# Optimization experiments

Measured on AMD Instinct MI355X. Metric: run time of the kernel, lower is better.

Reference implementation:

```python
import jax, jax.numpy as jnp
import numpy as np

B = 65536   # batch
F = 256     # FeatureDim
E = 8       # experts_num
D = 64      # ExpertOutDim
EPS = 1e-5  # BatchNorm eps (eval mode: running stats)


def _bn(x, g, be, m, v):
    # BatchNorm1d in eval mode
    return (x - m) * jax.lax.rsqrt(v + EPS) * g + be


def setup_inputs() -> dict:
    key = jax.random.key(0)
    ks = jax.random.split(key, 40)
    r = lambda i, s: jax.random.normal(ks[i], s, dtype=jnp.float32) * 0.05
    u = lambda i, s: jax.random.uniform(ks[i], s, dtype=jnp.float32)
    return dict(
        signal_em=jax.random.normal(ks[0], (B, F), dtype=jnp.float32),
        muti_em=jax.random.normal(ks[1], (B, F), dtype=jnp.float32),
        similarity=jax.random.uniform(ks[2], (B,), dtype=jnp.float32),
        w=u(3, ()), b=u(4, ()),
        ps_W=r(5, (F, 256)), ps_b=r(6, (256,)), ps_g=u(7, (256,)), ps_be=r(8, (256,)), ps_m=r(9, (256,)), ps_v=u(10, (256,)) + 0.5,
        pm_W=r(11, (F, 256)), pm_b=r(12, (256,)), pm_g=u(13, (256,)), pm_be=r(14, (256,)), pm_m=r(15, (256,)), pm_v=u(16, (256,)) + 0.5,
        c1_W=r(17, (2 * F, 64)), c1_b=r(18, (64,)), c1_g=u(19, (64,)), c1_be=r(20, (64,)), c1_m=r(21, (64,)), c1_v=u(22, (64,)) + 0.5,
        c2_W=r(23, (64, 64)), c2_b=r(24, (64,)), c2_g=u(25, (64,)), c2_be=r(26, (64,)), c2_m=r(27, (64,)), c2_v=u(28, (64,)) + 0.5,
        c3_W=r(29, (64, 2)), c3_b=r(30, (2,)),
        e_W1=r(31, (E, 2 * F, 256)), e_b1=r(32, (E, 256)),
        e_W2=r(33, (E, 256, D)), e_b2=r(34, (E, D)),
        s_W1=r(35, (E, E)), s_b1=r(36, (E,)), s_W2=r(37, (E, E)), s_b2=r(38, (E,)),
    )


def reference(signal_em, muti_em, similarity, w, b,
              ps_W, ps_b, ps_g, ps_be, ps_m, ps_v,
              pm_W, pm_b, pm_g, pm_be, pm_m, pm_v,
              c1_W, c1_b, c1_g, c1_be, c1_m, c1_v,
              c2_W, c2_b, c2_g, c2_be, c2_m, c2_v,
              c3_W, c3_b,
              e_W1, e_b1, e_W2, e_b2,
              s_W1, s_b1, s_W2, s_b2):
    sim_weight = similarity[:, None] * w + b                        # [B,1]
    sig = jax.nn.relu(_bn(signal_em @ ps_W + ps_b, ps_g, ps_be, ps_m, ps_v))
    sig = sim_weight * sig
    mut = jax.nn.relu(_bn(muti_em @ pm_W + pm_b, pm_g, pm_be, pm_m, pm_v))
    temp = jnp.concatenate([sig, mut], axis=1)                      # [B, 512]

    # classifier head (dropout = identity in eval mode)
    h = jax.nn.relu(_bn(temp @ c1_W + c1_b, c1_g, c1_be, c1_m, c1_v))
    h = jax.nn.relu(_bn(h @ c2_W + c2_b, c2_g, c2_be, c2_m, c2_v))
    pre_score = h @ c3_W + c3_b                                     # [B,2]

    # all E experts as one batched GEMM (Expert_net has dropout p=0)
    eh = jax.nn.relu(jnp.einsum('bf,efh->beh', temp, e_W1) + e_b1)  # [B,E,256]
    eo = jax.nn.relu(jnp.einsum('beh,ehd->bed', eh, e_W2) + e_b2)   # [B,E,64]

    # SE-style gating: avg/max pool over expert-out dim (kernel==D -> scalar)
    att_ave = eo.mean(axis=-1)                                      # [B,E]
    att_max = eo.max(axis=-1)                                       # [B,E]
    senet = lambda x: jax.nn.gelu(x @ s_W1 + s_b1, approximate=False) @ s_W2 + s_b2
    wts = jax.nn.sigmoid(senet(att_ave) + senet(att_max))           # [B,E]

    gate_out = jnp.einsum('bed,be->bd', eo, wts)                    # [B,D]
    return (gate_out, pre_score)
```

## Files before the change

### kernel.cpp

```cpp
#include <hip/hip_runtime.h>
#include <math.h>

using u32 = unsigned int;
using u16 = unsigned short;
typedef __attribute__((ext_vector_type(4))) float f4;
typedef __attribute__((ext_vector_type(4))) u32 u4;
typedef __attribute__((ext_vector_type(2))) u32 u2;
typedef __attribute__((ext_vector_type(8))) __bf16 b8;

union U4B8 { u4 u; b8 b; };

__device__ __forceinline__ u16 f2b(float x) {
  u32 u = __float_as_uint(x);
  u32 r = (u + 0x7FFFu + ((u >> 16) & 1u)) >> 16;
  return (u16)r;
}
__device__ __forceinline__ u32 pack2(float a, float b) { return (u32)f2b(a) | ((u32)f2b(b) << 16); }
__device__ __forceinline__ f4 mfma16(b8 a, b8 b, f4 c) {
  return __builtin_amdgcn_mfma_f32_16x16x32_bf16(a, b, c, 0, 0, 0);
}

#define FENCE() asm volatile("" ::: "memory")
#define RAWBAR() do { FENCE(); __builtin_amdgcn_s_barrier(); FENCE(); __builtin_amdgcn_sched_barrier(0); } while (0)
#define VMW(nlit) do { asm volatile("s_waitcnt vmcnt(" nlit ")" ::: "memory"); __builtin_amdgcn_sched_barrier(0); } while (0)
#define LGKM0() do { asm volatile("s_waitcnt lgkmcnt(0)" ::: "memory"); __builtin_amdgcn_sched_barrier(0); } while (0)
#define LBAR() do { LGKM0(); __builtin_amdgcn_s_barrier(); FENCE(); __builtin_amdgcn_sched_barrier(0); } while (0)

template <int NB>
__device__ __forceinline__ void gstage(const u16* g, u16* l, int t) {
#pragma unroll
  for (int i = 0; i < NB; i += 8192) {
    __builtin_amdgcn_global_load_lds(
        (__attribute__((address_space(1))) u32*)(g + (i >> 1) + t * 8),
        (__attribute__((address_space(3))) u32*)(l + (i >> 1) + ((t >> 6) << 9)),
        16, 0, 0);
  }
}

__global__ void prep_kernel(
    const float* __restrict__ ps_W, const float* __restrict__ ps_b, const float* __restrict__ ps_g,
    const float* __restrict__ ps_be, const float* __restrict__ ps_m, const float* __restrict__ ps_v,
    const float* __restrict__ pm_W, const float* __restrict__ pm_b, const float* __restrict__ pm_g,
    const float* __restrict__ pm_be, const float* __restrict__ pm_m, const float* __restrict__ pm_v,
    const float* __restrict__ c1_W, const float* __restrict__ c1_b, const float* __restrict__ c1_g,
    const float* __restrict__ c1_be, const float* __restrict__ c1_m, const float* __restrict__ c1_v,
    const float* __restrict__ c2_W, const float* __restrict__ c2_b, const float* __restrict__ c2_g,
    const float* __restrict__ c2_be, const float* __restrict__ c2_m, const float* __restrict__ c2_v,
    const float* __restrict__ e_W1, const float* __restrict__ e_W2,
    u16* __restrict__ w1t, u16* __restrict__ w2t, u16* __restrict__ pst, u16* __restrict__ pmt,
    u16* __restrict__ c1t, u16* __restrict__ c2t, float* __restrict__ fold)
{
  int i0 = blockIdx.x * blockDim.x + threadIdx.x;
  int stride = gridDim.x * blockDim.x;
  for (int idx = i0; idx < 8 * 256 * 512; idx += stride) {
    int e = idx >> 17; int rem = idx & 131071;
    int s = rem >> 14; int rem2 = rem & 16383;
    int n = rem2 >> 6; int q = rem2 & 63;
    int k = s * 64 + (q ^ ((n & 7) << 3));
    w1t[idx] = f2b(e_W1[e * 131072 + k * 256 + n]);
  }
  for (int idx = i0; idx < 8 * 64 * 256; idx += stride) {
    int e = idx >> 14; int rem = idx & 16383;
    int d = rem >> 8; int q = rem & 255;
    int h = q ^ ((d & 7) << 3);
    w2t[idx] = f2b(e_W2[e * 16384 + h * 64 + d]);
  }
  for (int idx = i0; idx < 65536; idx += stride) {
    int s = idx >> 14; int rem = idx & 16383;
    int n = rem >> 6, q = rem & 63;
    int k = s * 64 + (q ^ ((n & 7) << 3));
    pst[idx] = f2b(ps_W[k * 256 + n]);
    pmt[idx] = f2b(pm_W[k * 256 + n]);
  }
  for (int idx = i0; idx < 64 * 512; idx += stride) {
    int n = idx >> 9, q = idx & 511;
    int k = q ^ ((n & 7) << 3);
    c1t[idx] = f2b(c1_W[k * 64 + n]);
  }
  for (int idx = i0; idx < 64 * 64; idx += stride) {
    int n = idx >> 6, k = idx & 63;
    c2t[idx] = f2b(c2_W[k * 64 + n]);
  }
  for (int idx = i0; idx < 256; idx += stride) {
    float a = ps_g[idx] * rsqrtf(ps_v[idx] + 1e-5f);
    fold[idx] = a; fold[256 + idx] = (ps_b[idx] - ps_m[idx]) * a + ps_be[idx];
    float a2 = pm_g[idx] * rsqrtf(pm_v[idx] + 1e-5f);
    fold[512 + idx] = a2; fold[768 + idx] = (pm_b[idx] - pm_m[idx]) * a2 + pm_be[idx];
  }
  for (int idx = i0; idx < 64; idx += stride) {
    float a = c1_g[idx] * rsqrtf(c1_v[idx] + 1e-5f);
    fold[1024 + idx] = a; fold[1088 + idx] = (c1_b[idx] - c1_m[idx]) * a + c1_be[idx];
    float a2 = c2_g[idx] * rsqrtf(c2_v[idx] + 1e-5f);
    fold[1152 + idx] = a2; fold[1216 + idx] = (c2_b[idx] - c2_m[idx]) * a2 + c2_be[idx];
  }
}

__global__ __launch_bounds__(512, 4) void k1_kernel(
    const float* __restrict__ sig, const float* __restrict__ mut,
    const float* __restrict__ simil, const float* __restrict__ wS, const float* __restrict__ bS,
    const u16* __restrict__ pst, const u16* __restrict__ pmt,
    const float* __restrict__ fold, u16* __restrict__ temp)
{
  extern __shared__ __align__(16) u16 smk[];
  const int t = threadIdx.x, w = t >> 6, l = t & 63;
  const int lr = l & 15, lk = (l >> 4) * 8, lv = (l >> 4) * 4;
  const int xoru = (l & 7) << 3;
  const int rg = w >> 1, cg = w & 1;
  const int half = blockIdx.y;
  const float* X = half ? mut : sig;
  const u16* Wt = half ? pmt : pst;
  const int rb = blockIdx.x;
  const int rg0 = rb * 64;
  const f4 ZF = {0.f, 0.f, 0.f, 0.f};
  const int myrow = rg * 16 + lr;

  f4 xr[16];
  {
    const float* xp = X + (rg0 + myrow) * 256 + lk;
#pragma unroll
    for (int c = 0; c < 8; ++c) {
      xr[2 * c]     = *(const f4*)(xp + c * 32);
      xr[2 * c + 1] = *(const f4*)(xp + c * 32 + 4);
    }
  }
  float swv = 1.f;
  if (half == 0) swv = simil[rg0 + myrow] * wS[0] + bS[0];
  gstage<32768>(Wt, smk, t);
  b8 af[8];
#pragma unroll
  for (int c = 0; c < 8; ++c) {
    U4B8 tmp;
    tmp.u[0] = pack2(xr[2 * c][0], xr[2 * c][1]);
    tmp.u[1] = pack2(xr[2 * c][2], xr[2 * c][3]);
    tmp.u[2] = pack2(xr[2 * c + 1][0], xr[2 * c + 1][1]);
    tmp.u[3] = pack2(xr[2 * c + 1][2], xr[2 * c + 1][3]);
    af[c] = tmp.b;
  }

  f4 acc[8];
#pragma unroll
  for (int i = 0; i < 8; ++i) acc[i] = ZF;

#define K1P(P, STG) do { \
    VMW("0"); RAWBAR(); \
    STG; \
    __builtin_amdgcn_s_setprio(1); \
    _Pragma("unroll") for (int kk = 0; kk < 2; ++kk) { \
      b8 bf[8]; \
      _Pragma("unroll") for (int nf = 0; nf < 8; ++nf) \
        bf[nf] = *(const b8*)(smk + ((P) & 1) * 16384 + (cg * 128 + nf * 16 + lr) * 64 + ((kk * 32 + lk) ^ xoru)); \
      _Pragma("unroll") for (int nf = 0; nf < 8; ++nf) \
        acc[nf] = mfma16(bf[nf], af[(P) * 2 + kk], acc[nf]); \
    } \
    __builtin_amdgcn_s_setprio(0); \
  } while (0)

  K1P(0, gstage<32768>(Wt + 16384, smk + 16384, t));
  K1P(1, gstage<32768>(Wt + 32768, smk, t));
  K1P(2, gstage<32768>(Wt + 49152, smk + 16384, t));
  K1P(3, (void)0);
#undef K1P

#pragma unroll
  for (int nf = 0; nf < 8; ++nf) {
    int col = cg * 128 + nf * 16 + lv;
    const f4 al = *(const f4*)(fold + half * 512 + col);
    const f4 be = *(const f4*)(fold + half * 512 + 256 + col);
    float v0 = fmaxf(acc[nf][0] * al[0] + be[0], 0.f) * swv;
    float v1 = fmaxf(acc[nf][1] * al[1] + be[1], 0.f) * swv;
    float v2 = fmaxf(acc[nf][2] * al[2] + be[2], 0.f) * swv;
    float v3 = fmaxf(acc[nf][3] * al[3] + be[3], 0.f) * swv;
    u2 pv; pv[0] = pack2(v0, v1); pv[1] = pack2(v2, v3);
    int st = col >> 6;
    int kin = col & 63;
    int q = kin ^ ((myrow & 7) << 3);
    *(u2*)(smk + st * 4096 + myrow * 64 + q) = pv;
  }
  LBAR();
  {
    u16* dst = temp + (rb >> 1) * 65536 + half * 32768 + (rb & 1) * 4096;
#pragma unroll
    for (int st = 0; st < 4; ++st) {
      u4 v = *(const u4*)(smk + st * 4096 + t * 8);
      *(u4*)(dst + st * 8192 + t * 8) = v;
    }
  }
}

__global__ __launch_bounds__(512, 2) void k2_kernel(
    u16* __restrict__ temp, const u16* __restrict__ w1t, const u16* __restrict__ w2t,
    const u16* __restrict__ c1t, const u16* __restrict__ c2t,
    const float* __restrict__ fold,
    const float* __restrict__ c3W, const float* __restrict__ c3B,
    const float* __restrict__ eb1, const float* __restrict__ eb2,
    const float* __restrict__ sW1, const float* __restrict__ sB1,
    const float* __restrict__ sW2, const float* __restrict__ sB2,
    float* __restrict__ outp)
{
  extern __shared__ __align__(16) u16 sm[];
  u16* smW  = sm;
  u16* smE  = sm + 32768;
  u16* smR2 = sm + 49152;
  float* attA  = (float*)(sm + 65536);
  float* attM  = attA + 1024;
  float* wtsb  = attM + 1024;
  float* c3sm  = wtsb + 1024;
  float* eb1sm = c3sm + 136;
  float* eb2sm = eb1sm + 2048;

  const int t = threadIdx.x, w = t >> 6, l = t & 63;
  const int lr = l & 15, lk = (l >> 4) * 8, lv = (l >> 4) * 4;
  const int xoru = (l & 7) << 3;
  const int rg = w >> 1, cg = w & 1;
  const int rg0 = blockIdx.x * 128;
  const f4 ZF = {0.f, 0.f, 0.f, 0.f};
  u16* tempE = temp + blockIdx.x * 65536;

  b8 af[16][2];

#define AFLOAD(R) { \
    _Pragma("unroll") for (int c8 = 0; c8 < 8; ++c8) { \
      _Pragma("unroll") for (int mi = 0; mi < 2; ++mi) \
        af[(R) * 8 + c8][mi] = *(const b8*)(smE + (c8 >> 1) * 8192 + (rg * 32 + mi * 16 + lr) * 64 + ((((c8 & 1) * 32) + lk) ^ xoru)); \
    } }

  {
    f4 rEb1 = *(const f4*)(eb1 + t * 4);
    f4 rEb2 = ZF; if (t < 128) rEb2 = *(const f4*)(eb2 + t * 4);
    float rC3 = 0.f; if (t < 128) rC3 = c3W[t]; else if (t < 130) rC3 = c3B[t - 128];
    u4 rC2 = *(const u4*)(c2t + (t >> 3) * 64 + (t & 7) * 8);

    gstage<65536>(tempE, smE, t);
    gstage<65536>(c1t, smW, t);
    *(f4*)(eb1sm + t * 4) = rEb1;
    if (t < 128) *(f4*)(eb2sm + t * 4) = rEb2;
    if (t < 130) c3sm[t] = rC3;
    VMW("8"); RAWBAR();
    AFLOAD(0);
    asm volatile("s_waitcnt lgkmcnt(0)" ::: "memory");
    RAWBAR();
    gstage<65536>(tempE + 32768, smE, t);
    VMW("8"); RAWBAR();
    f4 ah[2][2] = {{ZF, ZF}, {ZF, ZF}};
#define HPART(R) { \
    __builtin_amdgcn_s_setprio(1); \
    _Pragma("unroll") for (int c8 = 0; c8 < 8; ++c8) { \
      _Pragma("unroll") for (int nf = 0; nf < 2; ++nf) { \
        b8 ch = *(const b8*)(smW + (cg * 32 + nf * 16 + lr) * 512 + ((((R) * 8 + c8) * 32 + lk) ^ xoru)); \
        _Pragma("unroll") for (int mi = 0; mi < 2; ++mi) \
          ah[nf][mi] = mfma16(ch, af[(R) * 8 + c8][mi], ah[nf][mi]); \
      } } \
    __builtin_amdgcn_s_setprio(0); }
    HPART(0)
    VMW("0"); RAWBAR();
    AFLOAD(1);
    HPART(1)
#undef HPART
    asm volatile("s_waitcnt lgkmcnt(0)" ::: "memory");
    RAWBAR();
    u16* h1b = smE;
    u16* c2sm = smR2;
    u16* h2b = smR2 + 4608;
#pragma unroll
    for (int nf = 0; nf < 2; ++nf) {
      int col = cg * 32 + nf * 16 + lv;
      const f4 av1 = *(const f4*)(fold + 1024 + col);
      const f4 bv1 = *(const f4*)(fold + 1088 + col);
#pragma unroll
      for (int mi = 0; mi < 2; ++mi) {
        int row = rg * 32 + mi * 16 + lr;
        u2 pv;
        pv[0] = pack2(fmaxf(ah[nf][mi][0] * av1[0] + bv1[0], 0.f), fmaxf(ah[nf][mi][1] * av1[1] + bv1[1], 0.f));
        pv[1] = pack2(fmaxf(ah[nf][mi][2] * av1[2] + bv1[2], 0.f), fmaxf(ah[nf][mi][3] * av1[3] + bv1[3], 0.f));
        *(u2*)(h1b + row * 72 + col) = pv;
      }
    }
    *(u4*)(c2sm + (t >> 3) * 72 + (t & 7) * 8) = rC2;
    LBAR();
    f4 a2[2][2] = {{ZF, ZF}, {ZF, ZF}};
#pragma unroll
    for (int kk = 0; kk < 2; ++kk) {
      b8 hf[2], cf[2];
#pragma unroll
      for (int mi = 0; mi < 2; ++mi)
        hf[mi] = *(const b8*)(h1b + (rg * 32 + mi * 16 + lr) * 72 + kk * 32 + lk);
#pragma unroll
      for (int nf = 0; nf < 2; ++nf)
        cf[nf] = *(const b8*)(c2sm + (cg * 32 + nf * 16 + lr) * 72 + kk * 32 + lk);
#pragma unroll
      for (int mi = 0; mi < 2; ++mi)
#pragma unroll
        for (int nf = 0; nf < 2; ++nf)
          a2[mi][nf] = mfma16(cf[nf], hf[mi], a2[mi][nf]);
    }
#pragma unroll
    for (int nf = 0; nf < 2; ++nf) {
      int col = cg * 32 + nf * 16 + lv;
      const f4 av2 = *(const f4*)(fold + 1152 + col);
      const f4 bv2 = *(const f4*)(fold + 1216 + col);
#pragma unroll
      for (int mi = 0; mi < 2; ++mi) {
        int row = rg * 32 + mi * 16 + lr;
        u2 pv;
        pv[0] = pack2(fmaxf(a2[mi][nf][0] * av2[0] + bv2[0], 0.f), fmaxf(a2[mi][nf][1] * av2[1] + bv2[1], 0.f));
        pv[1] = pack2(fmaxf(a2[mi][nf][2] * av2[2] + bv2[2], 0.f), fmaxf(a2[mi][nf][3] * av2[3] + bv2[3], 0.f));
        *(u2*)(h2b + row * 72 + col) = pv;
      }
    }
    LBAR();
    if (t < 256) {
      int row = t >> 1, c = t & 1;
      float s_ = c3sm[128 + c];
#pragma unroll
      for (int j = 0; j < 8; ++j) {
        u4 hv = *(const u4*)(h2b + row * 72 + j * 8);
#pragma unroll
        for (int q = 0; q < 4; ++q) {
          float lo = __uint_as_float(hv[q] << 16);
          float hi = __uint_as_float(hv[q] & 0xffff0000u);
          s_ += lo * c3sm[(j * 8 + q * 2) * 2 + c];
          s_ += hi * c3sm[(j * 8 + q * 2 + 1) * 2 + c];
        }
      }
      outp[4194304 + (rg0 + row) * 2 + c] = s_;
    }
    RAWBAR();
    gstage<32768>(w1t, smW, t);
  }

#define MPH(P, NW, ...) do { \
    VMW(NW); RAWBAR(); \
    __VA_ARGS__; \
    __builtin_amdgcn_s_setprio(1); \
    _Pragma("unroll") for (int kk = 0; kk < 2; ++kk) { \
      b8 bfA[4], bfB[4]; \
      _Pragma("unroll") for (int nf = 0; nf < 4; ++nf) \
        bfA[nf] = *(const b8*)(smW + ((P) & 1) * 16384 + (cg * 64 + nf * 16 + lr) * 64 + ((kk * 32 + lk) ^ xoru)); \
      _Pragma("unroll") for (int nf = 0; nf < 4; ++nf) \
        bfB[nf] = *(const b8*)(smW + ((P) & 1) * 16384 + 8192 + (cg * 64 + nf * 16 + lr) * 64 + ((kk * 32 + lk) ^ xoru)); \
      _Pragma("unroll") for (int nf = 0; nf < 4; ++nf) \
        _Pragma("unroll") for (int mi = 0; mi < 2; ++mi) \
          acc[nf][mi] = mfma16(bfA[nf], af[(P) * 2 + kk][mi], acc[nf][mi]); \
      _Pragma("unroll") for (int nf = 0; nf < 4; ++nf) \
        _Pragma("unroll") for (int mi = 0; mi < 2; ++mi) \
          acc[4 + nf][mi] = mfma16(bfB[nf], af[(P) * 2 + kk][mi], acc[4 + nf][mi]); \
    } \
    __builtin_amdgcn_s_setprio(0); \
  } while (0)

#define EHEPI(E, H) { \
    _Pragma("unroll") for (int nf = 0; nf < 4; ++nf) { \
      int colL = cg * 64 + nf * 16 + lv; \
      const f4 bv = *(const f4*)(eb1sm + (E) * 256 + (H) * 128 + colL); \
      _Pragma("unroll") for (int mi = 0; mi < 2; ++mi) { \
        int row = rg * 32 + mi * 16 + lr; \
        f4 a_ = acc[(H) * 4 + nf][mi]; \
        u2 pv; \
        pv[0] = pack2(fmaxf(a_[0] + bv[0], 0.f), fmaxf(a_[1] + bv[1], 0.f)); \
        pv[1] = pack2(fmaxf(a_[2] + bv[2], 0.f), fmaxf(a_[3] + bv[3], 0.f)); \
        *(u2*)(smE + row * 128 + (colL ^ xoru)) = pv; \
      } } }

#define G2PASS(P) do { \
    __builtin_amdgcn_s_setprio(1); \
    _Pragma("unroll") for (int kk = 0; kk < 4; ++kk) { \
      b8 wf[2], ef[2]; \
      _Pragma("unroll") for (int nf = 0; nf < 2; ++nf) \
        wf[nf] = *(const b8*)(smR2 + (cg * 32 + nf * 16 + lr) * 256 + (((P) * 128 + kk * 32 + lk) ^ xoru)); \
      _Pragma("unroll") for (int mi = 0; mi < 2; ++mi) \
        ef[mi] = *(const b8*)(smE + (rg * 32 + mi * 16 + lr) * 128 + ((kk * 32 + lk) ^ xoru)); \
      _Pragma("unroll") for (int mi = 0; mi < 2; ++mi) \
        _Pragma("unroll") for (int nf = 0; nf < 2; ++nf) \
          e2[mi][nf] = mfma16(wf[nf], ef[mi], e2[mi][nf]); \
    } \
    __builtin_amdgcn_s_setprio(0); \
  } while (0)

#define EXPERT(E, NWP0, NWG2) { \
    const u16* w1E = w1t + (E) * 131072; \
    const u16* w1N = w1t + (((E) < 7 ? (E) + 1 : 7)) * 131072; \
    f4 acc[8][2]; \
    _Pragma("unroll") for (int nf = 0; nf < 8; ++nf) \
      _Pragma("unroll") for (int mi = 0; mi < 2; ++mi) acc[nf][mi] = ZF; \
    MPH(0, NWP0, gstage<32768>(w1E + 1 * 16384, smW + 16384, t)); \
    MPH(1, "0",  gstage<32768>(w1E + 2 * 16384, smW, t)); \
    MPH(2, "0",  gstage<32768>(w1E + 3 * 16384, smW + 16384, t)); \
    MPH(3, "0",  gstage<32768>(w1E + 4 * 16384, smW, t)); \
    MPH(4, "0",  gstage<32768>(w1E + 5 * 16384, smW + 16384, t)); \
    MPH(5, "0",  gstage<32768>(w1E + 6 * 16384, smW, t)); \
    MPH(6, "0",  { gstage<32768>(w1E + 7 * 16384, smW + 16384, t); \
                   gstage<32768>(w2t + (E) * 16384, smR2, t); }); \
    MPH(7, "4",  { if ((E) < 7) gstage<32768>(w1t + ((E) + 1) * 131072, smW, t); }); \
    EHEPI(E, 0) \
    VMW(NWG2); LBAR(); \
    f4 e2[2][2]; \
    e2[0][0] = ZF; e2[0][1] = ZF; e2[1][0] = ZF; e2[1][1] = ZF; \
    G2PASS(0); \
    RAWBAR(); \
    EHEPI(E, 1) \
    LBAR(); \
    G2PASS(1); \
    RAWBAR(); \
     \
    _Pragma("unroll") for (int nf = 0; nf < 2; ++nf) { \
      int d0 = cg * 32 + nf * 16 + lv; \
      const f4 bv2 = *(const f4*)(eb2sm + (E) * 64 + d0); \
      _Pragma("unroll") for (int mi = 0; mi < 2; ++mi) { \
        int row = rg * 32 + mi * 16 + lr; \
        u2 pv; \
        pv[0] = pack2(fmaxf(e2[mi][nf][0] + bv2[0], 0.f), fmaxf(e2[mi][nf][1] + bv2[1], 0.f)); \
        pv[1] = pack2(fmaxf(e2[mi][nf][2] + bv2[2], 0.f), fmaxf(e2[mi][nf][3] + bv2[3], 0.f)); \
        *(u2*)(smE + row * 72 + d0) = pv; \
      } } \
    LBAR(); \
    {  \
      int prow = t >> 2, pd = (t & 3) * 16; \
      const u16* er = smE + prow * 72 + pd; \
      u4 qa = *(const u4*)(er); u4 qb = *(const u4*)(er + 8); \
      float sum = 0.f, mx = 0.f; \
      _Pragma("unroll") for (int q = 0; q < 4; ++q) { \
        float a0 = __uint_as_float(qa[q] << 16), a1 = __uint_as_float(qa[q] & 0xffff0000u); \
        float b0 = __uint_as_float(qb[q] << 16), b1 = __uint_as_float(qb[q] & 0xffff0000u); \
        sum += a0 + a1 + b0 + b1; \
        mx = fmaxf(mx, fmaxf(fmaxf(a0, a1), fmaxf(b0, b1))); \
      } \
      sum += __shfl_xor(sum, 1); sum += __shfl_xor(sum, 2); \
      mx = fmaxf(mx, __shfl_xor(mx, 1)); mx = fmaxf(mx, __shfl_xor(mx, 2)); \
      if ((t & 3) == 0) { attA[prow * 8 + (E)] = sum * (1.f / 64.f); attM[prow * 8 + (E)] = mx; } \
      u16* wsE = tempE + (E) * 8192 + prow * 64 + pd; \
      *(u4*)(wsE) = qa; *(u4*)(wsE + 8) = qb; \
    } \
  }

  EXPERT(0, "0", "4")
  EXPERT(1, "2", "4")
  EXPERT(2, "2", "4")
  EXPERT(3, "2", "4")
  EXPERT(4, "2", "4")
  EXPERT(5, "2", "4")
  EXPERT(6, "2", "4")
  EXPERT(7, "2", "0")
#undef EXPERT
#undef MPH
#undef EHEPI
#undef G2PASS

  VMW("0");
  LBAR();
  if (t < 128) {
    float xa[8], xm[8], ga[8], gm[8];
#pragma unroll
    for (int j = 0; j < 8; ++j) { xa[j] = attA[t * 8 + j]; xm[j] = attM[t * 8 + j]; }
#pragma unroll
    for (int j = 0; j < 8; ++j) {
      float a1 = sB1[j], a2 = sB1[j];
#pragma unroll
      for (int i = 0; i < 8; ++i) { float wv = sW1[i * 8 + j]; a1 += xa[i] * wv; a2 += xm[i] * wv; }
      ga[j] = 0.5f * a1 * (1.f + erff(a1 * 0.70710678118654752f));
      gm[j] = 0.5f * a2 * (1.f + erff(a2 * 0.70710678118654752f));
    }
#pragma unroll
    for (int j = 0; j < 8; ++j) {
      float o1 = sB2[j], o2 = sB2[j];
#pragma unroll
      for (int i = 0; i < 8; ++i) { float wv = sW2[i * 8 + j]; o1 += ga[i] * wv; o2 += gm[i] * wv; }
      float z = o1 + o2;
      wtsb[t * 8 + j] = 1.f / (1.f + expf(-z));
    }
  }
  LBAR();
  {
    int grow = t >> 2, gd0 = (t & 3) * 16;
    float wv[8];
#pragma unroll
    for (int e2_ = 0; e2_ < 8; ++e2_) wv[e2_] = wtsb[grow * 8 + e2_];
    float g[16];
#pragma unroll
    for (int j = 0; j < 16; ++j) g[j] = 0.f;
#pragma unroll
    for (int e2_ = 0; e2_ < 8; ++e2_) {
      const u16* wsE = tempE + e2_ * 8192 + grow * 64 + gd0;
      u4 qa = *(const u4*)(wsE); u4 qb = *(const u4*)(wsE + 8);
#pragma unroll
      for (int q = 0; q < 4; ++q) {
        g[2 * q + 0] += wv[e2_] * __uint_as_float(qa[q] << 16);
        g[2 * q + 1] += wv[e2_] * __uint_as_float(qa[q] & 0xffff0000u);
        g[8 + 2 * q + 0] += wv[e2_] * __uint_as_float(qb[q] << 16);
        g[8 + 2 * q + 1] += wv[e2_] * __uint_as_float(qb[q] & 0xffff0000u);
      }
    }
    float* op = outp + (rg0 + grow) * 64 + gd0;
    f4 o0 = {g[0], g[1], g[2], g[3]}, o1 = {g[4], g[5], g[6], g[7]};
    f4 o2 = {g[8], g[9], g[10], g[11]}, o3 = {g[12], g[13], g[14], g[15]};
    *(f4*)op = o0; *(f4*)(op + 4) = o1; *(f4*)(op + 8) = o2; *(f4*)(op + 12) = o3;
  }
}

extern "C" void kernel_launch(void* const* d_in, const int* in_sizes, int n_in,
                              void* d_out, int out_size, void* d_ws, size_t ws_size,
                              hipStream_t stream) {
  const float* signal = (const float*)d_in[0];
  const float* muti   = (const float*)d_in[1];
  const float* simil  = (const float*)d_in[2];
  const float* wS     = (const float*)d_in[3];
  const float* bS     = (const float*)d_in[4];
  const float* ps_W = (const float*)d_in[5];  const float* ps_b = (const float*)d_in[6];
  const float* ps_g = (const float*)d_in[7];  const float* ps_be = (const float*)d_in[8];
  const float* ps_m = (const float*)d_in[9];  const float* ps_v = (const float*)d_in[10];
  const float* pm_W = (const float*)d_in[11]; const float* pm_b = (const float*)d_in[12];
  const float* pm_g = (const float*)d_in[13]; const float* pm_be = (const float*)d_in[14];
  const float* pm_m = (const float*)d_in[15]; const float* pm_v = (const float*)d_in[16];
  const float* c1_W = (const float*)d_in[17]; const float* c1_b = (const float*)d_in[18];
  const float* c1_g = (const float*)d_in[19]; const float* c1_be = (const float*)d_in[20];
  const float* c1_m = (const float*)d_in[21]; const float* c1_v = (const float*)d_in[22];
  const float* c2_W = (const float*)d_in[23]; const float* c2_b = (const float*)d_in[24];
  const float* c2_g = (const float*)d_in[25]; const float* c2_be = (const float*)d_in[26];
  const float* c2_m = (const float*)d_in[27]; const float* c2_v = (const float*)d_in[28];
  const float* c3_W = (const float*)d_in[29]; const float* c3_b = (const float*)d_in[30];
  const float* e_W1 = (const float*)d_in[31]; const float* e_b1 = (const float*)d_in[32];
  const float* e_W2 = (const float*)d_in[33]; const float* e_b2 = (const float*)d_in[34];
  const float* s_W1 = (const float*)d_in[35]; const float* s_b1 = (const float*)d_in[36];
  const float* s_W2 = (const float*)d_in[37]; const float* s_b2 = (const float*)d_in[38];

  char* ws = (char*)d_ws;
  u16* temp = (u16*)ws;
  u16* w1t  = (u16*)(ws + 67108864);
  u16* w2t  = (u16*)(ws + 69206016);
  u16* pst  = (u16*)(ws + 69468160);
  u16* pmt  = (u16*)(ws + 69599232);
  u16* c1t  = (u16*)(ws + 69730304);
  u16* c2t  = (u16*)(ws + 69795840);
  float* fold = (float*)(ws + 69804032);
  float* outp = (float*)d_out;

  prep_kernel<<<dim3(512), dim3(256), 0, stream>>>(
      ps_W, ps_b, ps_g, ps_be, ps_m, ps_v, pm_W, pm_b, pm_g, pm_be, pm_m, pm_v,
      c1_W, c1_b, c1_g, c1_be, c1_m, c1_v, c2_W, c2_b, c2_g, c2_be, c2_m, c2_v,
      e_W1, e_W2, w1t, w2t, pst, pmt, c1t, c2t, fold);
  k1_kernel<<<dim3(1024, 2), dim3(512), 65536, stream>>>(
      signal, muti, simil, wS, bS, pst, pmt, fold, temp);
  k2_kernel<<<dim3(512), dim3(512), 154144, stream>>>(
      temp, w1t, w2t, c1t, c2t, fold, c3_W, c3_b, e_b1, e_b2, s_W1, s_b1, s_W2, s_b2, outp);
}
```

Before: 268.0 us.

## Overlap expert weight conversion with k1 and restructure expert second GEMM epilogue

Moves the bf16 conversion of the expert W1/W2 weights out of the prep kernel into an extra grid slice of k1, so it runs alongside the projection GEMM instead of serially before it. In k2, both halves of the expert hidden activation are written to shared memory before a single 256-deep second GEMM, which removes a barrier-separated two-pass schedule. The avg/max pooling is now computed straight from the MFMA accumulators using cross-lane shuffles plus shared-memory atomics, dropping a shared-memory round trip and one barrier. The trade-off is reuse of the W1 staging buffer, different vmcnt wait counts, and atomics on the attention buffers.

```diff
diff --git a/kernel.cpp b/kernel.cpp
--- a/kernel.cpp
+++ b/kernel.cpp
@@ -46,25 +46,11 @@
     const float* __restrict__ c1_be, const float* __restrict__ c1_m, const float* __restrict__ c1_v,
     const float* __restrict__ c2_W, const float* __restrict__ c2_b, const float* __restrict__ c2_g,
     const float* __restrict__ c2_be, const float* __restrict__ c2_m, const float* __restrict__ c2_v,
-    const float* __restrict__ e_W1, const float* __restrict__ e_W2,
-    u16* __restrict__ w1t, u16* __restrict__ w2t, u16* __restrict__ pst, u16* __restrict__ pmt,
+    u16* __restrict__ pst, u16* __restrict__ pmt,
     u16* __restrict__ c1t, u16* __restrict__ c2t, float* __restrict__ fold)
 {
   int i0 = blockIdx.x * blockDim.x + threadIdx.x;
   int stride = gridDim.x * blockDim.x;
-  for (int idx = i0; idx < 8 * 256 * 512; idx += stride) {
-    int e = idx >> 17; int rem = idx & 131071;
-    int s = rem >> 14; int rem2 = rem & 16383;
-    int n = rem2 >> 6; int q = rem2 & 63;
-    int k = s * 64 + (q ^ ((n & 7) << 3));
-    w1t[idx] = f2b(e_W1[e * 131072 + k * 256 + n]);
-  }
-  for (int idx = i0; idx < 8 * 64 * 256; idx += stride) {
-    int e = idx >> 14; int rem = idx & 16383;
-    int d = rem >> 8; int q = rem & 255;
-    int h = q ^ ((d & 7) << 3);
-    w2t[idx] = f2b(e_W2[e * 16384 + h * 64 + d]);
-  }
   for (int idx = i0; idx < 65536; idx += stride) {
     int s = idx >> 14; int rem = idx & 16383;
     int n = rem >> 6, q = rem & 63;
@@ -99,10 +85,31 @@
     const float* __restrict__ sig, const float* __restrict__ mut,
     const float* __restrict__ simil, const float* __restrict__ wS, const float* __restrict__ bS,
     const u16* __restrict__ pst, const u16* __restrict__ pmt,
-    const float* __restrict__ fold, u16* __restrict__ temp)
+    const float* __restrict__ fold, u16* __restrict__ temp,
+    const float* __restrict__ e_W1, const float* __restrict__ e_W2,
+    u16* __restrict__ w1t, u16* __restrict__ w2t)
 {
   extern __shared__ __align__(16) u16 smk[];
-  const int t = threadIdx.x, w = t >> 6, l = t & 63;
+  const int t = threadIdx.x;
+  if (blockIdx.y == 2) {
+    int i0 = blockIdx.x * 512 + t;
+    const int stride = 1024 * 512;
+    for (int idx = i0; idx < 8 * 256 * 512; idx += stride) {
+      int e = idx >> 17; int rem = idx & 131071;
+      int s = rem >> 14; int rem2 = rem & 16383;
+      int n = rem2 >> 6; int q = rem2 & 63;
+      int k = s * 64 + (q ^ ((n & 7) << 3));
+      w1t[idx] = f2b(e_W1[e * 131072 + k * 256 + n]);
+    }
+    for (int idx = i0; idx < 8 * 64 * 256; idx += stride) {
+      int e = idx >> 14; int rem = idx & 16383;
+      int d = rem >> 8; int q = rem & 255;
+      int h = q ^ ((d & 7) << 3);
+      w2t[idx] = f2b(e_W2[e * 16384 + h * 64 + d]);
+    }
+    return;
+  }
+  const int w = t >> 6, l = t & 63;
   const int lr = l & 15, lk = (l >> 4) * 8, lv = (l >> 4) * 4;
   const int xoru = (l & 7) << 3;
   const int rg = w >> 1, cg = w & 1;
@@ -225,6 +232,7 @@
     } }
 
   {
+    for (int z = t; z < 2048; z += 512) attA[z] = 0.f;
     f4 rEb1 = *(const f4*)(eb1 + t * 4);
     f4 rEb2 = ZF; if (t < 128) rEb2 = *(const f4*)(eb2 + t * 4);
     float rC3 = 0.f; if (t < 128) rC3 = c3W[t]; else if (t < 130) rC3 = c3B[t - 128];
@@ -348,7 +356,7 @@
     __builtin_amdgcn_s_setprio(0); \
   } while (0)
 
-#define EHEPI(E, H) { \
+#define EHEPI(E, H, DST) { \
     _Pragma("unroll") for (int nf = 0; nf < 4; ++nf) { \
       int colL = cg * 64 + nf * 16 + lv; \
       const f4 bv = *(const f4*)(eb1sm + (E) * 256 + (H) * 128 + colL); \
@@ -358,17 +366,18 @@
         u2 pv; \
         pv[0] = pack2(fmaxf(a_[0] + bv[0], 0.f), fmaxf(a_[1] + bv[1], 0.f)); \
         pv[1] = pack2(fmaxf(a_[2] + bv[2], 0.f), fmaxf(a_[3] + bv[3], 0.f)); \
-        *(u2*)(smE + row * 128 + (colL ^ xoru)) = pv; \
+        *(u2*)((DST) + row * 128 + (colL ^ xoru)) = pv; \
       } } }
 
-#define G2PASS(P) do { \
+#define G2ALL() do { \
     __builtin_amdgcn_s_setprio(1); \
-    _Pragma("unroll") for (int kk = 0; kk < 4; ++kk) { \
+    _Pragma("unroll") for (int kq = 0; kq < 8; ++kq) { \
+      const u16* ebase = (kq < 4) ? smE : (smW + 16384); \
       b8 wf[2], ef[2]; \
       _Pragma("unroll") for (int nf = 0; nf < 2; ++nf) \
-        wf[nf] = *(const b8*)(smR2 + (cg * 32 + nf * 16 + lr) * 256 + (((P) * 128 + kk * 32 + lk) ^ xoru)); \
+        wf[nf] = *(const b8*)(smR2 + (cg * 32 + nf * 16 + lr) * 256 + ((kq * 32 + lk) ^ xoru)); \
       _Pragma("unroll") for (int mi = 0; mi < 2; ++mi) \
-        ef[mi] = *(const b8*)(smE + (rg * 32 + mi * 16 + lr) * 128 + ((kk * 32 + lk) ^ xoru)); \
+        ef[mi] = *(const b8*)(ebase + (rg * 32 + mi * 16 + lr) * 128 + ((((kq & 3) * 32) + lk) ^ xoru)); \
       _Pragma("unroll") for (int mi = 0; mi < 2; ++mi) \
         _Pragma("unroll") for (int nf = 0; nf < 2; ++nf) \
           e2[mi][nf] = mfma16(wf[nf], ef[mi], e2[mi][nf]); \
@@ -378,7 +387,6 @@
 
 #define EXPERT(E, NWP0, NWG2) { \
     const u16* w1E = w1t + (E) * 131072; \
-    const u16* w1N = w1t + (((E) < 7 ? (E) + 1 : 7)) * 131072; \
     f4 acc[8][2]; \
     _Pragma("unroll") for (int nf = 0; nf < 8; ++nf) \
       _Pragma("unroll") for (int mi = 0; mi < 2; ++mi) acc[nf][mi] = ZF; \
@@ -391,66 +399,60 @@
     MPH(6, "0",  { gstage<32768>(w1E + 7 * 16384, smW + 16384, t); \
                    gstage<32768>(w2t + (E) * 16384, smR2, t); }); \
     MPH(7, "4",  { if ((E) < 7) gstage<32768>(w1t + ((E) + 1) * 131072, smW, t); }); \
-    EHEPI(E, 0) \
-    VMW(NWG2); LBAR(); \
+    EHEPI(E, 0, smE) \
+    RAWBAR();  \
+    EHEPI(E, 1, smW + 16384) \
+    VMW(NWG2); LBAR();  \
     f4 e2[2][2]; \
     e2[0][0] = ZF; e2[0][1] = ZF; e2[1][0] = ZF; e2[1][1] = ZF; \
-    G2PASS(0); \
-    RAWBAR(); \
-    EHEPI(E, 1) \
-    LBAR(); \
-    G2PASS(1); \
-    RAWBAR(); \
+    G2ALL(); \
      \
-    _Pragma("unroll") for (int nf = 0; nf < 2; ++nf) { \
-      int d0 = cg * 32 + nf * 16 + lv; \
-      const f4 bv2 = *(const f4*)(eb2sm + (E) * 64 + d0); \
-      _Pragma("unroll") for (int mi = 0; mi < 2; ++mi) { \
-        int row = rg * 32 + mi * 16 + lr; \
-        u2 pv; \
-        pv[0] = pack2(fmaxf(e2[mi][nf][0] + bv2[0], 0.f), fmaxf(e2[mi][nf][1] + bv2[1], 0.f)); \
-        pv[1] = pack2(fmaxf(e2[mi][nf][2] + bv2[2], 0.f), fmaxf(e2[mi][nf][3] + bv2[3], 0.f)); \
-        *(u2*)(smE + row * 72 + d0) = pv; \
-      } } \
-    LBAR(); \
-    {  \
-      int prow = t >> 2, pd = (t & 3) * 16; \
-      const u16* er = smE + prow * 72 + pd; \
-      u4 qa = *(const u4*)(er); u4 qb = *(const u4*)(er + 8); \
-      float sum = 0.f, mx = 0.f; \
-      _Pragma("unroll") for (int q = 0; q < 4; ++q) { \
-        float a0 = __uint_as_float(qa[q] << 16), a1 = __uint_as_float(qa[q] & 0xffff0000u); \
-        float b0 = __uint_as_float(qb[q] << 16), b1 = __uint_as_float(qb[q] & 0xffff0000u); \
-        sum += a0 + a1 + b0 + b1; \
-        mx = fmaxf(mx, fmaxf(fmaxf(a0, a1), fmaxf(b0, b1))); \
+    _Pragma("unroll") for (int mi = 0; mi < 2; ++mi) { \
+      int row = rg * 32 + mi * 16 + lr; \
+      float s_ = 0.f, mx = 0.f; \
+      _Pragma("unroll") for (int nf = 0; nf < 2; ++nf) { \
+        int d0 = cg * 32 + nf * 16 + lv; \
+        const f4 bv2 = *(const f4*)(eb2sm + (E) * 64 + d0); \
+        float v0 = fmaxf(e2[mi][nf][0] + bv2[0], 0.f); \
+        float v1 = fmaxf(e2[mi][nf][1] + bv2[1], 0.f); \
+        float v2 = fmaxf(e2[mi][nf][2] + bv2[2], 0.f); \
+        float v3 = fmaxf(e2[mi][nf][3] + bv2[3], 0.f); \
+        s_ += v0 + v1 + v2 + v3; \
+        mx = fmaxf(mx, fmaxf(fmaxf(v0, v1), fmaxf(v2, v3))); \
+        u2 pv; pv[0] = pack2(v0, v1); pv[1] = pack2(v2, v3); \
+        *(u2*)(tempE + (E) * 8192 + row * 64 + d0) = pv; \
       } \
-      sum += __shfl_xor(sum, 1); sum += __shfl_xor(sum, 2); \
-      mx = fmaxf(mx, __shfl_xor(mx, 1)); mx = fmaxf(mx, __shfl_xor(mx, 2)); \
-      if ((t & 3) == 0) { attA[prow * 8 + (E)] = sum * (1.f / 64.f); attM[prow * 8 + (E)] = mx; } \
-      u16* wsE = tempE + (E) * 8192 + prow * 64 + pd; \
-      *(u4*)(wsE) = qa; *(u4*)(wsE + 8) = qb; \
+      s_ += __shfl_xor(s_, 16); s_ += __shfl_xor(s_, 32); \
+      mx = fmaxf(mx, __shfl_xor(mx, 16)); mx = fmaxf(mx, __shfl_xor(mx, 32)); \
+      if (l < 16) { \
+        atomicAdd(attA + row * 8 + (E), s_); \
+        atomicMax((unsigned int*)(attM + row * 8 + (E)), __float_as_uint(mx)); \
+      } \
     } \
   }
 
   EXPERT(0, "0", "4")
-  EXPERT(1, "2", "4")
-  EXPERT(2, "2", "4")
-  EXPERT(3, "2", "4")
-  EXPERT(4, "2", "4")
-  EXPERT(5, "2", "4")
-  EXPERT(6, "2", "4")
-  EXPERT(7, "2", "0")
+  EXPERT(1, "4", "4")
+  EXPERT(2, "4", "4")
+  EXPERT(3, "4", "4")
+  EXPERT(4, "4", "4")
+  EXPERT(5, "4", "4")
+  EXPERT(6, "4", "4")
+  EXPERT(7, "4", "0")
 #undef EXPERT
 #undef MPH
 #undef EHEPI
-#undef G2PASS
+#undef G2ALL
 
   VMW("0");
   LBAR();
   if (t < 128) {
     float xa[8], xm[8], ga[8], gm[8];
 #pragma unroll
-    for (int j = 0; j < 8; ++j) { xa[j] = attA[t * 8 + j]; xm[j] = attM[t * 8 + j]; }
+    for (int j = 0; j < 8; ++j) {
+      xa[j] = attA[t * 8 + j] * 0.015625f;
+      xm[j] = attM[t * 8 + j];
+    }
 #pragma unroll
     for (int j = 0; j < 8; ++j) {
       float a1 = sB1[j], a2 = sB1[j];
@@ -533,12 +535,12 @@
   float* fold = (float*)(ws + 69804032);
   float* outp = (float*)d_out;
 
-  prep_kernel<<<dim3(512), dim3(256), 0, stream>>>(
+  prep_kernel<<<dim3(256), dim3(256), 0, stream>>>(
       ps_W, ps_b, ps_g, ps_be, ps_m, ps_v, pm_W, pm_b, pm_g, pm_be, pm_m, pm_v,
       c1_W, c1_b, c1_g, c1_be, c1_m, c1_v, c2_W, c2_b, c2_g, c2_be, c2_m, c2_v,
-      e_W1, e_W2, w1t, w2t, pst, pmt, c1t, c2t, fold);
-  k1_kernel<<<dim3(1024, 2), dim3(512), 65536, stream>>>(
-      signal, muti, simil, wS, bS, pst, pmt, fold, temp);
+      pst, pmt, c1t, c2t, fold);
+  k1_kernel<<<dim3(1024, 3), dim3(512), 65536, stream>>>(
+      signal, muti, simil, wS, bS, pst, pmt, fold, temp, e_W1, e_W2, w1t, w2t);
   k2_kernel<<<dim3(512), dim3(512), 154144, stream>>>(
       temp, w1t, w2t, c1t, c2t, fold, c3_W, c3_b, e_b1, e_b2, s_W1, s_b1, s_W2, s_b2, outp);
 }
```

Result: faster. 261.7 us (-2.3%).
